# Kernel optimization log

Hardware: AMD Instinct MI355X
Metric: run time of the kernel (lower is better)

The kernel has to match this reference:

```python
import jax, jax.numpy as jnp
import numpy as np

K_WEIGHT = 1.5  # K passed to w() in the original forward
B_EXP = 2.5     # default exponent b in w()


def setup_inputs() -> dict:
    key = jax.random.key(0)
    k1, k2 = jax.random.split(key)
    B, H, D = 4096, 128, 64
    pred = jax.random.normal(k1, (B, H, D), dtype=jnp.float32)
    targ = jax.random.normal(k2, (B, H, D), dtype=jnp.float32)
    return {"pred": pred, "targ": targ}


def reference(pred, targ):
    # pred, targ: [B, H, D]
    B, H, D = pred.shape
    diff = pred - targ                      # loss2
    loss = diff * diff                      # (pred - targ)**2
    # loss3[:, 1:] = diff[:, :-1]; loss3[:, 0] = 0
    loss3 = jnp.concatenate([jnp.zeros_like(diff[:, :1]), diff[:, :-1]], axis=1)
    loss1 = jnp.abs(diff - loss3)           # temporal-difference loss

    # t_i = number of nonzero entries in targ[i, :, 1]
    t = jnp.sum(targ[:, :, 1] != 0, axis=1)              # [B] int
    t_f = t.astype(pred.dtype)
    # w(t, T=H, K=1.5, b=2.5) = 1 + (K-1) * (t/(H-1))**b
    wgt = 1.0 + (K_WEIGHT - 1.0) * (t_f / (H - 1)) ** B_EXP  # [B]

    idx = t - 1
    idx = jnp.where(idx < 0, H - 1, idx)    # mimic torch negative indexing (t=0 -> -1 -> last)

    total = loss + loss1                     # [B, H, D]
    # gather row at index t-1 per sample: [B, D]
    row = jnp.take_along_axis(total, idx[:, None, None], axis=1)[:, 0, :]
    per_sample = wgt * jnp.sum(row, axis=1)  # masked[i, t-1, :] = wgt, summed over H,D
    weighted_loss = jnp.mean(per_sample)
    return weighted_loss
```

## Files before the change

### kernel.cpp

```cpp
#include <hip/hip_runtime.h>
#include <math.h>


#define H_DIM 128
#define D_DIM 64

__global__ __launch_bounds__(256) void wsl_stage1(
    const float* __restrict__ pred,
    const float* __restrict__ targ,
    float* __restrict__ partials,
    float invB)
{
    const int wave = threadIdx.x >> 6;
    const int lane = threadIdx.x & 63;
    const int sA   = blockIdx.x * 8 + wave * 2;
    const int sB   = sA + 1;
    const long long baseA = (long long)sA * (H_DIM * D_DIM);
    const long long baseB = (long long)sB * (H_DIM * D_DIM);

    const float cA0 = targ[baseA + (long long)lane * D_DIM + 1];
    const float cA1 = targ[baseA + (long long)(lane + 64) * D_DIM + 1];
    const float cB0 = targ[baseB + (long long)lane * D_DIM + 1];
    const float cB1 = targ[baseB + (long long)(lane + 64) * D_DIM + 1];
    const float pA_c = pred[baseA + 127 * D_DIM + lane];
    const float tA_c = targ[baseA + 127 * D_DIM + lane];
    const float pA_p = pred[baseA + 126 * D_DIM + lane];
    const float tA_p = targ[baseA + 126 * D_DIM + lane];
    const float pB_c = pred[baseB + 127 * D_DIM + lane];
    const float tB_c = targ[baseB + 127 * D_DIM + lane];
    const float pB_p = pred[baseB + 126 * D_DIM + lane];
    const float tB_p = targ[baseB + 126 * D_DIM + lane];

    const int tA = __popcll(__ballot(cA0 != 0.0f)) + __popcll(__ballot(cA1 != 0.0f));
    const int tB = __popcll(__ballot(cB0 != 0.0f)) + __popcll(__ballot(cB1 != 0.0f));

    float dcurA, dprevA, dcurB, dprevB;
    if (tA == H_DIM) {
        dcurA = pA_c - tA_c;  dprevA = pA_p - tA_p;
    } else {
        int idx = tA - 1; if (idx < 0) idx = H_DIM - 1;
        const long long off = baseA + (long long)idx * D_DIM + lane;
        dcurA = pred[off] - targ[off];
        dprevA = (idx >= 1) ? (pred[off - D_DIM] - targ[off - D_DIM]) : 0.0f;
    }
    if (tB == H_DIM) {
        dcurB = pB_c - tB_c;  dprevB = pB_p - tB_p;
    } else {
        int idx = tB - 1; if (idx < 0) idx = H_DIM - 1;
        const long long off = baseB + (long long)idx * D_DIM + lane;
        dcurB = pred[off] - targ[off];
        dprevB = (idx >= 1) ? (pred[off - D_DIM] - targ[off - D_DIM]) : 0.0f;
    }

    float sA_ = dcurA * dcurA + fabsf(dcurA - dprevA);
    float sB_ = dcurB * dcurB + fabsf(dcurB - dprevB);

    #pragma unroll
    for (int sh = 32; sh >= 1; sh >>= 1) {
        sA_ += __shfl_down(sA_, sh, 64);
        sB_ += __shfl_down(sB_, sh, 64);
    }

    if (lane == 0) {
        const float fA = (float)tA / (float)(H_DIM - 1);
        const float fB = (float)tB / (float)(H_DIM - 1);
        const float wA = 1.0f + 0.5f * powf(fA, 2.5f);
        const float wB = 1.0f + 0.5f * powf(fB, 2.5f);
        partials[blockIdx.x * 4 + wave] = (wA * sA_ + wB * sB_) * invB;
    }
}

__global__ __launch_bounds__(256) void wsl_stage2(
    const float* __restrict__ partials,
    float* __restrict__ out,
    int n)
{
    __shared__ float s[256];
    const int tid = threadIdx.x;
    float acc = 0.0f;
    #pragma unroll
    for (int k = 0; k < 8; ++k) {
        const int j = tid + k * 256;
        if (j < n) acc += partials[j];
    }
    s[tid] = acc;
    __syncthreads();
    #pragma unroll
    for (int st = 128; st >= 1; st >>= 1) {
        if (tid < st) s[tid] += s[tid + st];
        __syncthreads();
    }
    if (tid == 0) out[0] = s[0];
}

extern "C" void kernel_launch(void* const* d_in, const int* in_sizes, int n_in,
                              void* d_out, int out_size, void* d_ws, size_t ws_size,
                              hipStream_t stream)
{
    const float* pred = (const float*)d_in[0];
    const float* targ = (const float*)d_in[1];
    float* out = (float*)d_out;

    const int B = in_sizes[0] / (H_DIM * D_DIM);
    const int nblocks = B / 8;
    const int npart = nblocks * 4;

    float* partials = (float*)d_ws;

    wsl_stage1<<<nblocks, 256, 0, stream>>>(pred, targ, partials, 1.0f / (float)B);
    wsl_stage2<<<1, 256, 0, stream>>>(partials, out, npart);
}
```

Measured before the change: 23.00 us.

## Fuse two-stage reduction into one kernel with last-block ticket

Merges the per-block partial kernel and the final reduction kernel into one launch. Each block writes its partials with device-scope atomics, then takes a ticket with an atomic counter, and the last block to arrive sums all partials. The ticket is never reset; the code instead takes it modulo nblocks, which assumes nblocks is a power of two. This removes a second kernel launch and its gap, at the cost of an atomic per block and a serialized tail in the last block.

```diff
diff --git a/kernel.cpp b/kernel.cpp
--- a/kernel.cpp
+++ b/kernel.cpp
@@ -5,18 +5,24 @@
 #define H_DIM 128
 #define D_DIM 64
 
-__global__ __launch_bounds__(256) void wsl_stage1(
+__global__ __launch_bounds__(256) void wsl_onepass(
     const float* __restrict__ pred,
     const float* __restrict__ targ,
     float* __restrict__ partials,
-    float invB)
+    unsigned int* __restrict__ ticket,
+    float* __restrict__ out,
+    float invB, int nblocks)
 {
-    const int wave = threadIdx.x >> 6;
-    const int lane = threadIdx.x & 63;
+    const int tid  = threadIdx.x;
+    const int wave = tid >> 6;
+    const int lane = tid & 63;
     const int sA   = blockIdx.x * 8 + wave * 2;
     const int sB   = sA + 1;
     const long long baseA = (long long)sA * (H_DIM * D_DIM);
     const long long baseB = (long long)sB * (H_DIM * D_DIM);
+
+    __shared__ unsigned int s_last;
+    __shared__ float sred[256];
 
     const float cA0 = targ[baseA + (long long)lane * D_DIM + 1];
     const float cA1 = targ[baseA + (long long)(lane + 64) * D_DIM + 1];
@@ -66,31 +72,34 @@
         const float fB = (float)tB / (float)(H_DIM - 1);
         const float wA = 1.0f + 0.5f * powf(fA, 2.5f);
         const float wB = 1.0f + 0.5f * powf(fB, 2.5f);
-        partials[blockIdx.x * 4 + wave] = (wA * sA_ + wB * sB_) * invB;
+        const float pv = (wA * sA_ + wB * sB_) * invB;
+        atomicExch(&partials[blockIdx.x * 4 + wave], pv);
     }
-}
+    asm volatile("s_waitcnt vmcnt(0)" ::: "memory");
+    __syncthreads();
 
-__global__ __launch_bounds__(256) void wsl_stage2(
-    const float* __restrict__ partials,
-    float* __restrict__ out,
-    int n)
-{
-    __shared__ float s[256];
-    const int tid = threadIdx.x;
-    float acc = 0.0f;
-    #pragma unroll
-    for (int k = 0; k < 8; ++k) {
-        const int j = tid + k * 256;
-        if (j < n) acc += partials[j];
+    if (tid == 0) {
+        const unsigned int rank = atomicAdd(ticket, 1u);
+        s_last = ((rank & (unsigned)(nblocks - 1)) == (unsigned)(nblocks - 1)) ? 1u : 0u;
     }
-    s[tid] = acc;
     __syncthreads();
-    #pragma unroll
-    for (int st = 128; st >= 1; st >>= 1) {
-        if (tid < st) s[tid] += s[tid + st];
+
+    if (s_last) {
+        const int n = nblocks * 4;
+        float acc = 0.0f;
+        for (int j = tid; j < n; j += 256) {
+            acc += __hip_atomic_load(&partials[j], __ATOMIC_RELAXED,
+                                     __HIP_MEMORY_SCOPE_AGENT);
+        }
+        sred[tid] = acc;
         __syncthreads();
+        #pragma unroll
+        for (int st = 128; st >= 1; st >>= 1) {
+            if (tid < st) sred[tid] += sred[tid + st];
+            __syncthreads();
+        }
+        if (tid == 0) out[0] = sred[0];
     }
-    if (tid == 0) out[0] = s[0];
 }
 
 extern "C" void kernel_launch(void* const* d_in, const int* in_sizes, int n_in,
@@ -103,10 +112,10 @@
 
     const int B = in_sizes[0] / (H_DIM * D_DIM);
     const int nblocks = B / 8;
-    const int npart = nblocks * 4;
 
-    float* partials = (float*)d_ws;
+    float* partials      = (float*)d_ws;
+    unsigned int* ticket = (unsigned int*)(partials + nblocks * 4);
 
-    wsl_stage1<<<nblocks, 256, 0, stream>>>(pred, targ, partials, 1.0f / (float)B);
-    wsl_stage2<<<1, 256, 0, stream>>>(partials, out, npart);
+    wsl_onepass<<<nblocks, 256, 0, stream>>>(
+        pred, targ, partials, ticket, out, 1.0f / (float)B, nblocks);
 }
```

Result: no change. 22.57 us (-1.9%).
